# Kernel tuning notes

Hardware: AMD Instinct MI355X
Metric: run time of the kernel (lower is better)

The kernel has to match this reference:

```python
import jax, jax.numpy as jnp
import numpy as np

B, H, S = 64, 1024, 512
MIN_VAL, MAX_VAL = -1.0, 1.0
EPS = 1e-8  # torch F.cosine_similarity default eps


def setup_inputs() -> dict:
    key = jax.random.key(0)
    k1, k2, k3 = jax.random.split(key, 3)
    tree_state = jax.random.normal(k1, (B, H), dtype=jnp.float32)
    seq_states = jax.random.normal(k2, (B, H, S), dtype=jnp.float32)
    # binary validity mask (float, as it is multiplied in)
    seq_mask = (jax.random.uniform(k3, (B, S)) < 0.9).astype(jnp.float32)
    return {"tree_state": tree_state, "seq_states": seq_states, "seq_mask": seq_mask}


def reference(tree_state, seq_states, seq_mask):
    # scan over the seq axis; carry h: (B, H)
    xs = (jnp.transpose(seq_states, (2, 0, 1)), seq_mask.T)  # (S,B,H), (S,B)

    def step(h, x):
        s, m = x  # s: (B,H), m: (B,)
        dot = jnp.sum(h * s, axis=-1)  # (B,)
        denom = jnp.maximum(
            jnp.linalg.norm(h, axis=-1) * jnp.linalg.norm(s, axis=-1), EPS
        )
        cos = (dot / denom)[:, None]  # (B,1)
        h_new = jnp.clip(h + (s - h * cos) * m[:, None], MIN_VAL, MAX_VAL)
        return h_new, None

    h, _ = jax.lax.scan(step, tree_state, xs)
    return h
```

## Files before the change

kernel.cpp:

```cpp
#include <hip/hip_runtime.h>


#define NB 64
#define NH 1024
#define NS 512

typedef float v4f __attribute__((ext_vector_type(4)));
typedef int v4i __attribute__((ext_vector_type(4)));

template <int N> struct ic { static constexpr int value = N; };

template <int CTRL>
__device__ __forceinline__ float dpp_add(float x) {
  int s = __builtin_amdgcn_update_dpp(0, __builtin_bit_cast(int, x), CTRL, 0xf,
                                      0xf, true);
  return x + __builtin_bit_cast(float, s);
}

__device__ __forceinline__ float readlane_f(float v, int lane) {
  return __builtin_bit_cast(
      float, __builtin_amdgcn_readlane(__builtin_bit_cast(int, v), lane));
}

__device__ __forceinline__ void wave_sum3(float& a, float& b, float& c) {
  a = dpp_add<0x111>(a); b = dpp_add<0x111>(b); c = dpp_add<0x111>(c);
  a = dpp_add<0x112>(a); b = dpp_add<0x112>(b); c = dpp_add<0x112>(c);
  a = dpp_add<0x114>(a); b = dpp_add<0x114>(b); c = dpp_add<0x114>(c);
  a = dpp_add<0x118>(a); b = dpp_add<0x118>(b); c = dpp_add<0x118>(c);
  a = dpp_add<0x142>(a); b = dpp_add<0x142>(b); c = dpp_add<0x142>(c);
  a = dpp_add<0x143>(a); b = dpp_add<0x143>(b); c = dpp_add<0x143>(c);
  a = readlane_f(a, 63);
  b = readlane_f(b, 63);
  c = readlane_f(c, 63);
}

#define GLD4(dst, p, OFFSTR)                                   \
  asm volatile("global_load_dwordx4 %0, %1, off" OFFSTR        \
               : "=v"(dst)                                     \
               : "v"(p))
#define GLD1(dst, p)                                           \
  asm volatile("global_load_dword %0, %1, off" : "=v"(dst) : "v"(p))

template <int IMM>
__device__ __forceinline__ void dsr128(v4f& d, unsigned a) {
  asm volatile("ds_read_b128 %[d], %[a] offset:%[o]"
               : [d] "=v"(d)
               : [a] "v"(a), [o] "n"(IMM));
}
template <int IMM>
__device__ __forceinline__ void dsw32(unsigned a, float v) {
  asm volatile("ds_write_b32 %[a], %[v] offset:%[o]" ::[a] "v"(a), [v] "v"(v),
               [o] "n"(IMM));
}
__device__ __forceinline__ void bld4(v4f& d, unsigned voff, v4i srsrc,
                                     unsigned so) {
  asm volatile("buffer_load_dwordx4 %[d], %[vo], %[rs], %[so] offen"
               : [d] "=v"(d)
               : [vo] "v"(voff), [rs] "s"(srsrc), [so] "s"(so));
}

#define VMW12(rg)                                                          \
  asm volatile("s_waitcnt vmcnt(12)"                                       \
               : "+v"((rg)[0]), "+v"((rg)[1]), "+v"((rg)[2]), "+v"((rg)[3]))
#define LGK0(sv)                                                           \
  asm volatile("s_waitcnt lgkmcnt(0)"                                      \
               : "+v"((sv)[0]), "+v"((sv)[1]), "+v"((sv)[2]), "+v"((sv)[3]))

template <int T>
__device__ __forceinline__ void read_issue(unsigned rb, v4f (&sv)[4]) {
  dsr128<T * 4096 + 0>(sv[0], rb);
  dsr128<T * 4096 + 1024>(sv[1], rb);
  dsr128<T * 4096 + 2048>(sv[2], rb);
  dsr128<T * 4096 + 3072>(sv[3], rb);
}

template <int S>
__device__ __forceinline__ void stage_write(unsigned wb, v4f (&rg)[4]) {
#define DSWUJ(u, j) dsw32<(j) * 4096 + 256 * S + 64 * (u)>(wb, rg[u][j])
  DSWUJ(0, 0); DSWUJ(0, 1); DSWUJ(0, 2); DSWUJ(0, 3);
  DSWUJ(1, 0); DSWUJ(1, 1); DSWUJ(1, 2); DSWUJ(1, 3);
  DSWUJ(2, 0); DSWUJ(2, 1); DSWUJ(2, 2); DSWUJ(2, 3);
  DSWUJ(3, 0); DSWUJ(3, 1); DSWUJ(3, 2); DSWUJ(3, 3);
#undef DSWUJ
}

__device__ __forceinline__ void stage_load(v4f (&rg)[4], unsigned voff,
                                           v4i srsrc, unsigned& so) {
  bld4(rg[0], voff, srsrc, so); so += 32768u;
  bld4(rg[1], voff, srsrc, so); so += 32768u;
  bld4(rg[2], voff, srsrc, so); so += 32768u;
  bld4(rg[3], voff, srsrc, so); so += 32768u;
}

__device__ __forceinline__ void compute_step(float (&h)[16],
                                             const v4f (&sv)[4]) {
  float d0 = 0.f, d1 = 0.f, d2 = 0.f, d3 = 0.f;
  float e0 = 0.f, e1 = 0.f, e2 = 0.f, e3 = 0.f;
  float f0 = 0.f, f1 = 0.f, f2 = 0.f, f3 = 0.f;
#pragma unroll
  for (int m = 0; m < 4; ++m) {
    const float s0 = sv[m][0], s1 = sv[m][1], s2 = sv[m][2], s3 = sv[m][3];
    d0 = fmaf(h[4 * m + 0], s0, d0);
    e0 = fmaf(h[4 * m + 0], h[4 * m + 0], e0);
    f0 = fmaf(s0, s0, f0);
    d1 = fmaf(h[4 * m + 1], s1, d1);
    e1 = fmaf(h[4 * m + 1], h[4 * m + 1], e1);
    f1 = fmaf(s1, s1, f1);
    d2 = fmaf(h[4 * m + 2], s2, d2);
    e2 = fmaf(h[4 * m + 2], h[4 * m + 2], e2);
    f2 = fmaf(s2, s2, f2);
    d3 = fmaf(h[4 * m + 3], s3, d3);
    e3 = fmaf(h[4 * m + 3], h[4 * m + 3], e3);
    f3 = fmaf(s3, s3, f3);
  }
  float dot = (d0 + d1) + (d2 + d3);
  float hh = (e0 + e1) + (e2 + e3);
  float ss = (f0 + f1) + (f2 + f3);
  wave_sum3(dot, hh, ss);
  const float p = fmaxf(hh * ss, 1e-16f);
  const float c = dot * __builtin_amdgcn_rsqf(p);
  const float a = 1.0f - c;
#pragma unroll
  for (int m = 0; m < 4; ++m) {
    h[4 * m + 0] =
        __builtin_amdgcn_fmed3f(fmaf(h[4 * m + 0], a, sv[m][0]), -1.0f, 1.0f);
    h[4 * m + 1] =
        __builtin_amdgcn_fmed3f(fmaf(h[4 * m + 1], a, sv[m][1]), -1.0f, 1.0f);
    h[4 * m + 2] =
        __builtin_amdgcn_fmed3f(fmaf(h[4 * m + 2], a, sv[m][2]), -1.0f, 1.0f);
    h[4 * m + 3] =
        __builtin_amdgcn_fmed3f(fmaf(h[4 * m + 3], a, sv[m][3]), -1.0f, 1.0f);
  }
}

__global__ __launch_bounds__(64, 1) void otsu_scan_kernel(
    const float* __restrict__ tree,
    const float* __restrict__ seq,
    const float* __restrict__ mask,
    float* __restrict__ out) {
  __shared__ float lds[2 * 16 * 1024];
  const int b = blockIdx.x;
  const int l = threadIdx.x;

  const float* hrow = tree + b * NH + 4 * l;
  v4f hv[4];
  GLD4(hv[0], hrow, "");
  GLD4(hv[1], hrow, " offset:1024");
  GLD4(hv[2], hrow, " offset:2048");
  GLD4(hv[3], hrow, " offset:3072");
  float m8[8];
  {
    const float* mp = mask + b * NS + l;
    GLD1(m8[0], mp);
    GLD1(m8[1], mp + 64);
    GLD1(m8[2], mp + 128);
    GLD1(m8[3], mp + 192);
    GLD1(m8[4], mp + 256);
    GLD1(m8[5], mp + 320);
    GLD1(m8[6], mp + 384);
    GLD1(m8[7], mp + 448);
  }
  asm volatile("s_waitcnt vmcnt(0)"
               : "+v"(hv[0]), "+v"(hv[1]), "+v"(hv[2]), "+v"(hv[3]),
                 "+v"(m8[0]), "+v"(m8[1]), "+v"(m8[2]), "+v"(m8[3]),
                 "+v"(m8[4]), "+v"(m8[5]), "+v"(m8[6]), "+v"(m8[7]));

  float h[16];
#pragma unroll
  for (int m = 0; m < 4; ++m) {
    h[4 * m + 0] = hv[m][0];
    h[4 * m + 1] = hv[m][1];
    h[4 * m + 2] = hv[m][2];
    h[4 * m + 3] = hv[m][3];
  }

  unsigned mbits = 0u;
#pragma unroll
  for (int i = 0; i < 8; ++i)
    if (m8[i] != 0.0f) mbits |= (1u << i);

  if (!(__builtin_amdgcn_readlane((int)mbits, 0) & 1)) {
#pragma unroll
    for (int i = 0; i < 16; ++i)
      h[i] = __builtin_amdgcn_fmed3f(h[i], -1.0f, 1.0f);
  }

  v4i srsrc;
  {
    const unsigned long long base =
        (unsigned long long)(seq + (size_t)b * NH * NS);
    srsrc[0] = (int)(unsigned)(base & 0xffffffffull);
    srsrc[1] = (int)(unsigned)(base >> 32);
    srsrc[2] = NH * NS * 4;
    srsrc[3] = 0x00020000;
  }
  const unsigned voff = (unsigned)((l >> 2) * 2048 + (l & 3) * 16);
  const unsigned lb = (unsigned)(unsigned long long)(&lds[0]);
  const unsigned rb0 = lb + 16u * (unsigned)l;
  const unsigned wb0 = lb + (unsigned)((l & 3) * 16384 + (l >> 2) * 4);
  unsigned so = 0u;

  v4f ring[8][4];
  v4f sval[2][4];

  stage_load(ring[0], voff, srsrc, so);
  stage_load(ring[1], voff, srsrc, so);
  stage_load(ring[2], voff, srsrc, so);
  stage_load(ring[3], voff, srsrc, so);
#define PSTEP(v)                                              \
  do {                                                        \
    VMW12(ring[(v) & 7]);                                     \
    stage_write<(v)>(wb0, ring[(v) & 7]);                     \
    stage_load(ring[((v) + 4) & 7], voff, srsrc, so);         \
    if ((v) == 11) so -= 2097088u;     \
  } while (0)
  PSTEP(0);  PSTEP(1);  PSTEP(2);  PSTEP(3);
  PSTEP(4);  PSTEP(5);  PSTEP(6);  PSTEP(7);
  PSTEP(8);  PSTEP(9);  PSTEP(10); PSTEP(11);
  PSTEP(12); PSTEP(13); PSTEP(14); PSTEP(15);
#undef PSTEP

  read_issue<0>(rb0, sval[0]);

  unsigned rb_cur = rb0;
  unsigned wb_cur = wb0 ^ 0x10000u;

#pragma unroll 1
  for (int g = 0; g < 32; ++g) {
    const int lbase = (16 * g) & 63;
    const int msh = g >> 2;
    auto step = [&](auto sc) {
      constexpr int S = decltype(sc)::value;
      LGK0(sval[S & 1]);
      if constexpr (S < 15) read_issue<S + 1>(rb_cur, sval[(S + 1) & 1]);
      const unsigned mw =
          (unsigned)__builtin_amdgcn_readlane((int)mbits, lbase + S);
      if ((mw >> msh) & 1u) compute_step(h, sval[S & 1]);
      VMW12(ring[S & 7]);
      stage_write<S>(wb_cur, ring[S & 7]);
      stage_load(ring[(S + 4) & 7], voff, srsrc, so);
      if constexpr (S == 11) { so -= 2097088u; }
      if constexpr (S == 15) { read_issue<0>(rb_cur ^ 0x10000u, sval[0]); }
    };
    step(ic<0>{});  step(ic<1>{});  step(ic<2>{});  step(ic<3>{});
    step(ic<4>{});  step(ic<5>{});  step(ic<6>{});  step(ic<7>{});
    step(ic<8>{});  step(ic<9>{});  step(ic<10>{}); step(ic<11>{});
    step(ic<12>{}); step(ic<13>{}); step(ic<14>{}); step(ic<15>{});
    rb_cur ^= 0x10000u;
    wb_cur ^= 0x10000u;
  }

  asm volatile("s_waitcnt vmcnt(0) lgkmcnt(0)" ::: "memory");

  float* orow = out + b * NH + 4 * l;
#pragma unroll
  for (int m = 0; m < 4; ++m) {
    float4 v;
    v.x = h[4 * m + 0];
    v.y = h[4 * m + 1];
    v.z = h[4 * m + 2];
    v.w = h[4 * m + 3];
    *(float4*)(orow + 256 * m) = v;
  }
}

extern "C" void kernel_launch(void* const* d_in, const int* in_sizes, int n_in,
                              void* d_out, int out_size, void* d_ws,
                              size_t ws_size, hipStream_t stream) {
  const float* tree = (const float*)d_in[0];
  const float* seq = (const float*)d_in[1];
  const float* mask = (const float*)d_in[2];
  float* out = (float*)d_out;
  otsu_scan_kernel<<<dim3(NB), dim3(64), 0, stream>>>(tree, seq, mask, out);
}
```

Measured before the change: 316.4 us.

## Split each batch row across four waves with LDS cross-wave reduction

Each block now runs four waves instead of one, and each wave owns a quarter of the hidden dimension (4 floats per lane instead of 16). The per-step dot and norm partials are reduced inside each wave with DPP, exchanged through LDS, and synchronised with a block barrier each step. Streaming now uses global loads instead of buffer loads, and the wait thresholds are adjusted. This aims to cut the per-wave serial compute and memory issue on the latency-bound scan, at the cost of a barrier and an extra LDS round trip on every sequence step.

```diff
diff --git a/kernel.cpp b/kernel.cpp
--- a/kernel.cpp
+++ b/kernel.cpp
@@ -6,7 +6,6 @@
 #define NS 512
 
 typedef float v4f __attribute__((ext_vector_type(4)));
-typedef int v4i __attribute__((ext_vector_type(4)));
 
 template <int N> struct ic { static constexpr int value = N; };
 
@@ -17,28 +16,18 @@
   return x + __builtin_bit_cast(float, s);
 }
 
-__device__ __forceinline__ float readlane_f(float v, int lane) {
-  return __builtin_bit_cast(
-      float, __builtin_amdgcn_readlane(__builtin_bit_cast(int, v), lane));
-}
-
-__device__ __forceinline__ void wave_sum3(float& a, float& b, float& c) {
+__device__ __forceinline__ void wave_red3_to63(float& a, float& b, float& c) {
   a = dpp_add<0x111>(a); b = dpp_add<0x111>(b); c = dpp_add<0x111>(c);
   a = dpp_add<0x112>(a); b = dpp_add<0x112>(b); c = dpp_add<0x112>(c);
   a = dpp_add<0x114>(a); b = dpp_add<0x114>(b); c = dpp_add<0x114>(c);
   a = dpp_add<0x118>(a); b = dpp_add<0x118>(b); c = dpp_add<0x118>(c);
   a = dpp_add<0x142>(a); b = dpp_add<0x142>(b); c = dpp_add<0x142>(c);
   a = dpp_add<0x143>(a); b = dpp_add<0x143>(b); c = dpp_add<0x143>(c);
-  a = readlane_f(a, 63);
-  b = readlane_f(b, 63);
-  c = readlane_f(c, 63);
-}
-
-#define GLD4(dst, p, OFFSTR)                                   \
-  asm volatile("global_load_dwordx4 %0, %1, off" OFFSTR        \
-               : "=v"(dst)                                     \
-               : "v"(p))
-#define GLD1(dst, p)                                           \
+}
+
+#define GLD4(dst, p) \
+  asm volatile("global_load_dwordx4 %0, %1, off" : "=v"(dst) : "v"(p))
+#define GLD1(dst, p) \
   asm volatile("global_load_dword %0, %1, off" : "=v"(dst) : "v"(p))
 
 template <int IMM>
@@ -52,102 +41,35 @@
   asm volatile("ds_write_b32 %[a], %[v] offset:%[o]" ::[a] "v"(a), [v] "v"(v),
                [o] "n"(IMM));
 }
-__device__ __forceinline__ void bld4(v4f& d, unsigned voff, v4i srsrc,
-                                     unsigned so) {
-  asm volatile("buffer_load_dwordx4 %[d], %[vo], %[rs], %[so] offen"
-               : [d] "=v"(d)
-               : [vo] "v"(voff), [rs] "s"(srsrc), [so] "s"(so));
-}
-
-#define VMW12(rg)                                                          \
-  asm volatile("s_waitcnt vmcnt(12)"                                       \
-               : "+v"((rg)[0]), "+v"((rg)[1]), "+v"((rg)[2]), "+v"((rg)[3]))
-#define LGK0(sv)                                                           \
-  asm volatile("s_waitcnt lgkmcnt(0)"                                      \
-               : "+v"((sv)[0]), "+v"((sv)[1]), "+v"((sv)[2]), "+v"((sv)[3]))
-
-template <int T>
-__device__ __forceinline__ void read_issue(unsigned rb, v4f (&sv)[4]) {
-  dsr128<T * 4096 + 0>(sv[0], rb);
-  dsr128<T * 4096 + 1024>(sv[1], rb);
-  dsr128<T * 4096 + 2048>(sv[2], rb);
-  dsr128<T * 4096 + 3072>(sv[3], rb);
-}
+
+#define VMW3(r) asm volatile("s_waitcnt vmcnt(3)" : "+v"(r))
+#define LGK0SV(sv) asm volatile("s_waitcnt lgkmcnt(0)" : "+v"(sv))
+#define LGK5PR(p0, p1, p2)                  \
+  asm volatile("s_waitcnt lgkmcnt(5)"       \
+               : "+v"(p0), "+v"(p1), "+v"(p2))
 
 template <int S>
-__device__ __forceinline__ void stage_write(unsigned wb, v4f (&rg)[4]) {
-#define DSWUJ(u, j) dsw32<(j) * 4096 + 256 * S + 64 * (u)>(wb, rg[u][j])
-  DSWUJ(0, 0); DSWUJ(0, 1); DSWUJ(0, 2); DSWUJ(0, 3);
-  DSWUJ(1, 0); DSWUJ(1, 1); DSWUJ(1, 2); DSWUJ(1, 3);
-  DSWUJ(2, 0); DSWUJ(2, 1); DSWUJ(2, 2); DSWUJ(2, 3);
-  DSWUJ(3, 0); DSWUJ(3, 1); DSWUJ(3, 2); DSWUJ(3, 3);
-#undef DSWUJ
-}
-
-__device__ __forceinline__ void stage_load(v4f (&rg)[4], unsigned voff,
-                                           v4i srsrc, unsigned& so) {
-  bld4(rg[0], voff, srsrc, so); so += 32768u;
-  bld4(rg[1], voff, srsrc, so); so += 32768u;
-  bld4(rg[2], voff, srsrc, so); so += 32768u;
-  bld4(rg[3], voff, srsrc, so); so += 32768u;
-}
-
-__device__ __forceinline__ void compute_step(float (&h)[16],
-                                             const v4f (&sv)[4]) {
-  float d0 = 0.f, d1 = 0.f, d2 = 0.f, d3 = 0.f;
-  float e0 = 0.f, e1 = 0.f, e2 = 0.f, e3 = 0.f;
-  float f0 = 0.f, f1 = 0.f, f2 = 0.f, f3 = 0.f;
-#pragma unroll
-  for (int m = 0; m < 4; ++m) {
-    const float s0 = sv[m][0], s1 = sv[m][1], s2 = sv[m][2], s3 = sv[m][3];
-    d0 = fmaf(h[4 * m + 0], s0, d0);
-    e0 = fmaf(h[4 * m + 0], h[4 * m + 0], e0);
-    f0 = fmaf(s0, s0, f0);
-    d1 = fmaf(h[4 * m + 1], s1, d1);
-    e1 = fmaf(h[4 * m + 1], h[4 * m + 1], e1);
-    f1 = fmaf(s1, s1, f1);
-    d2 = fmaf(h[4 * m + 2], s2, d2);
-    e2 = fmaf(h[4 * m + 2], h[4 * m + 2], e2);
-    f2 = fmaf(s2, s2, f2);
-    d3 = fmaf(h[4 * m + 3], s3, d3);
-    e3 = fmaf(h[4 * m + 3], h[4 * m + 3], e3);
-    f3 = fmaf(s3, s3, f3);
-  }
-  float dot = (d0 + d1) + (d2 + d3);
-  float hh = (e0 + e1) + (e2 + e3);
-  float ss = (f0 + f1) + (f2 + f3);
-  wave_sum3(dot, hh, ss);
-  const float p = fmaxf(hh * ss, 1e-16f);
-  const float c = dot * __builtin_amdgcn_rsqf(p);
-  const float a = 1.0f - c;
-#pragma unroll
-  for (int m = 0; m < 4; ++m) {
-    h[4 * m + 0] =
-        __builtin_amdgcn_fmed3f(fmaf(h[4 * m + 0], a, sv[m][0]), -1.0f, 1.0f);
-    h[4 * m + 1] =
-        __builtin_amdgcn_fmed3f(fmaf(h[4 * m + 1], a, sv[m][1]), -1.0f, 1.0f);
-    h[4 * m + 2] =
-        __builtin_amdgcn_fmed3f(fmaf(h[4 * m + 2], a, sv[m][2]), -1.0f, 1.0f);
-    h[4 * m + 3] =
-        __builtin_amdgcn_fmed3f(fmaf(h[4 * m + 3], a, sv[m][3]), -1.0f, 1.0f);
-  }
-}
-
-__global__ __launch_bounds__(64, 1) void otsu_scan_kernel(
+__device__ __forceinline__ void stage_write(unsigned wb, v4f rg) {
+  dsw32<0 * 4096 + 64 * S>(wb, rg[0]);
+  dsw32<1 * 4096 + 64 * S>(wb, rg[1]);
+  dsw32<2 * 4096 + 64 * S>(wb, rg[2]);
+  dsw32<3 * 4096 + 64 * S>(wb, rg[3]);
+}
+
+__global__ __launch_bounds__(256, 1) void otsu_scan_kernel(
     const float* __restrict__ tree,
     const float* __restrict__ seq,
     const float* __restrict__ mask,
     float* __restrict__ out) {
-  __shared__ float lds[2 * 16 * 1024];
+  __shared__ float lds[2 * 16 * 1024 + 64];
   const int b = blockIdx.x;
-  const int l = threadIdx.x;
-
-  const float* hrow = tree + b * NH + 4 * l;
-  v4f hv[4];
-  GLD4(hv[0], hrow, "");
-  GLD4(hv[1], hrow, " offset:1024");
-  GLD4(hv[2], hrow, " offset:2048");
-  GLD4(hv[3], hrow, " offset:3072");
+  const int tid = threadIdx.x;
+  const int w = tid >> 6;
+  const int l = tid & 63;
+
+  const float* hrow = tree + b * NH + 256 * w + 4 * l;
+  v4f h;
+  GLD4(h, hrow);
   float m8[8];
   {
     const float* mp = mask + b * NS + l;
@@ -161,18 +83,8 @@
     GLD1(m8[7], mp + 448);
   }
   asm volatile("s_waitcnt vmcnt(0)"
-               : "+v"(hv[0]), "+v"(hv[1]), "+v"(hv[2]), "+v"(hv[3]),
-                 "+v"(m8[0]), "+v"(m8[1]), "+v"(m8[2]), "+v"(m8[3]),
+               : "+v"(h), "+v"(m8[0]), "+v"(m8[1]), "+v"(m8[2]), "+v"(m8[3]),
                  "+v"(m8[4]), "+v"(m8[5]), "+v"(m8[6]), "+v"(m8[7]));
-
-  float h[16];
-#pragma unroll
-  for (int m = 0; m < 4; ++m) {
-    h[4 * m + 0] = hv[m][0];
-    h[4 * m + 1] = hv[m][1];
-    h[4 * m + 2] = hv[m][2];
-    h[4 * m + 3] = hv[m][3];
-  }
 
   unsigned mbits = 0u;
 #pragma unroll
@@ -181,49 +93,45 @@
 
   if (!(__builtin_amdgcn_readlane((int)mbits, 0) & 1)) {
 #pragma unroll
-    for (int i = 0; i < 16; ++i)
+    for (int i = 0; i < 4; ++i)
       h[i] = __builtin_amdgcn_fmed3f(h[i], -1.0f, 1.0f);
   }
 
-  v4i srsrc;
-  {
-    const unsigned long long base =
-        (unsigned long long)(seq + (size_t)b * NH * NS);
-    srsrc[0] = (int)(unsigned)(base & 0xffffffffull);
-    srsrc[1] = (int)(unsigned)(base >> 32);
-    srsrc[2] = NH * NS * 4;
-    srsrc[3] = 0x00020000;
-  }
-  const unsigned voff = (unsigned)((l >> 2) * 2048 + (l & 3) * 16);
+  const float* sp0 = seq + (size_t)b * NH * NS + (size_t)w * 131072 +
+                     (l >> 2) * 512 + (l & 3) * 4;
+  const float* sp = sp0;
   const unsigned lb = (unsigned)(unsigned long long)(&lds[0]);
-  const unsigned rb0 = lb + 16u * (unsigned)l;
-  const unsigned wb0 = lb + (unsigned)((l & 3) * 16384 + (l >> 2) * 4);
-  unsigned so = 0u;
-
-  v4f ring[8][4];
-  v4f sval[2][4];
-
-  stage_load(ring[0], voff, srsrc, so);
-  stage_load(ring[1], voff, srsrc, so);
-  stage_load(ring[2], voff, srsrc, so);
-  stage_load(ring[3], voff, srsrc, so);
-#define PSTEP(v)                                              \
-  do {                                                        \
-    VMW12(ring[(v) & 7]);                                     \
-    stage_write<(v)>(wb0, ring[(v) & 7]);                     \
-    stage_load(ring[((v) + 4) & 7], voff, srsrc, so);         \
-    if ((v) == 11) so -= 2097088u;     \
+  unsigned rb = lb + 1024u * (unsigned)w + 16u * (unsigned)l;
+  unsigned wbase =
+      lb + 16384u * (unsigned)(l & 3) + 1024u * (unsigned)w +
+      4u * (unsigned)(l >> 2);
+  const unsigned vp = lb + 131072u + 4u * (unsigned)w;
+  const unsigned pb = lb + 131072u;
+
+  v4f ring[8];
+  v4f sval[2];
+
+  GLD4(ring[0], sp); sp += 8192;
+  GLD4(ring[1], sp); sp += 8192;
+  GLD4(ring[2], sp); sp += 8192;
+  GLD4(ring[3], sp); sp += 8192;
+#define PCH(c)                                              \
+  do {                                                      \
+    VMW3(ring[(c) & 7]);                                    \
+    stage_write<(c)>(wbase, ring[(c) & 7]);                 \
+    if ((c) == 12) sp -= 131056;     \
+    GLD4(ring[((c) + 4) & 7], sp);                          \
+    sp += 8192;                                             \
   } while (0)
-  PSTEP(0);  PSTEP(1);  PSTEP(2);  PSTEP(3);
-  PSTEP(4);  PSTEP(5);  PSTEP(6);  PSTEP(7);
-  PSTEP(8);  PSTEP(9);  PSTEP(10); PSTEP(11);
-  PSTEP(12); PSTEP(13); PSTEP(14); PSTEP(15);
-#undef PSTEP
-
-  read_issue<0>(rb0, sval[0]);
-
-  unsigned rb_cur = rb0;
-  unsigned wb_cur = wb0 ^ 0x10000u;
+  PCH(0);  PCH(1);  PCH(2);  PCH(3);
+  PCH(4);  PCH(5);  PCH(6);  PCH(7);
+  PCH(8);  PCH(9);  PCH(10); PCH(11);
+  PCH(12); PCH(13); PCH(14); PCH(15);
+#undef PCH
+
+  dsr128<0>(sval[0], rb);
+
+  unsigned wb = wbase ^ 0x10000u;
 
 #pragma unroll 1
   for (int g = 0; g < 32; ++g) {
@@ -231,37 +139,72 @@
     const int msh = g >> 2;
     auto step = [&](auto sc) {
       constexpr int S = decltype(sc)::value;
-      LGK0(sval[S & 1]);
-      if constexpr (S < 15) read_issue<S + 1>(rb_cur, sval[(S + 1) & 1]);
+      LGK0SV(sval[S & 1]);
       const unsigned mw =
           (unsigned)__builtin_amdgcn_readlane((int)mbits, lbase + S);
-      if ((mw >> msh) & 1u) compute_step(h, sval[S & 1]);
-      VMW12(ring[S & 7]);
-      stage_write<S>(wb_cur, ring[S & 7]);
-      stage_load(ring[(S + 4) & 7], voff, srsrc, so);
-      if constexpr (S == 11) { so -= 2097088u; }
-      if constexpr (S == 15) { read_issue<0>(rb_cur ^ 0x10000u, sval[0]); }
+      const bool act = (mw >> msh) & 1u;
+      v4f pr0, pr1, pr2;
+      if (act) {
+        const v4f s = sval[S & 1];
+        float pd0 = h[0] * s[0]; pd0 = fmaf(h[1], s[1], pd0);
+        float pd1 = h[2] * s[2]; pd1 = fmaf(h[3], s[3], pd1);
+        float ph0 = h[0] * h[0]; ph0 = fmaf(h[1], h[1], ph0);
+        float ph1 = h[2] * h[2]; ph1 = fmaf(h[3], h[3], ph1);
+        float ps0 = s[0] * s[0]; ps0 = fmaf(s[1], s[1], ps0);
+        float ps1 = s[2] * s[2]; ps1 = fmaf(s[3], s[3], ps1);
+        float pd = pd0 + pd1, ph = ph0 + ph1, ps = ps0 + ps1;
+        wave_red3_to63(pd, ph, ps);
+        if (l == 63) {
+          dsw32<(S & 3) * 64 + 0>(vp, pd);
+          dsw32<(S & 3) * 64 + 16>(vp, ph);
+          dsw32<(S & 3) * 64 + 32>(vp, ps);
+        }
+        asm volatile("s_waitcnt lgkmcnt(0)" ::: "memory");
+      }
+      asm volatile("s_barrier" ::: "memory");
+      if (act) {
+        dsr128<(S & 3) * 64 + 0>(pr0, pb);
+        dsr128<(S & 3) * 64 + 16>(pr1, pb);
+        dsr128<(S & 3) * 64 + 32>(pr2, pb);
+      }
+      VMW3(ring[S & 7]);
+      stage_write<S>(wb, ring[S & 7]);
+      if constexpr (S == 12) sp = (g < 30) ? sp - 131056 : sp0;
+      GLD4(ring[(S + 4) & 7], sp);
+      sp += 8192;
+      if constexpr (S < 15) dsr128<(S + 1) * 4096>(sval[(S + 1) & 1], rb);
+      else                  dsr128<0>(sval[0], rb ^ 0x10000u);
+      if (act) {
+        LGK5PR(pr0, pr1, pr2);
+        float dot = (pr0[0] + pr0[1]) + (pr0[2] + pr0[3]);
+        float hh = (pr1[0] + pr1[1]) + (pr1[2] + pr1[3]);
+        float ss = (pr2[0] + pr2[1]) + (pr2[2] + pr2[3]);
+        const float p = fmaxf(hh * ss, 1e-16f);
+        const float c = dot * __builtin_amdgcn_rsqf(p);
+        const float a = 1.0f - c;
+        const v4f s = sval[S & 1];
+#pragma unroll
+        for (int i = 0; i < 4; ++i)
+          h[i] = __builtin_amdgcn_fmed3f(fmaf(h[i], a, s[i]), -1.0f, 1.0f);
+      }
     };
     step(ic<0>{});  step(ic<1>{});  step(ic<2>{});  step(ic<3>{});
     step(ic<4>{});  step(ic<5>{});  step(ic<6>{});  step(ic<7>{});
     step(ic<8>{});  step(ic<9>{});  step(ic<10>{}); step(ic<11>{});
     step(ic<12>{}); step(ic<13>{}); step(ic<14>{}); step(ic<15>{});
-    rb_cur ^= 0x10000u;
-    wb_cur ^= 0x10000u;
+    rb ^= 0x10000u;
+    wb ^= 0x10000u;
   }
 
   asm volatile("s_waitcnt vmcnt(0) lgkmcnt(0)" ::: "memory");
 
-  float* orow = out + b * NH + 4 * l;
-#pragma unroll
-  for (int m = 0; m < 4; ++m) {
-    float4 v;
-    v.x = h[4 * m + 0];
-    v.y = h[4 * m + 1];
-    v.z = h[4 * m + 2];
-    v.w = h[4 * m + 3];
-    *(float4*)(orow + 256 * m) = v;
-  }
+  float* orow = out + b * NH + 256 * w + 4 * l;
+  float4 v;
+  v.x = h[0];
+  v.y = h[1];
+  v.z = h[2];
+  v.w = h[3];
+  *(float4*)orow = v;
 }
 
 extern "C" void kernel_launch(void* const* d_in, const int* in_sizes, int n_in,
@@ -271,5 +214,5 @@
   const float* seq = (const float*)d_in[1];
   const float* mask = (const float*)d_in[2];
   float* out = (float*)d_out;
-  otsu_scan_kernel<<<dim3(NB), dim3(64), 0, stream>>>(tree, seq, mask, out);
-}
+  otsu_scan_kernel<<<dim3(NB), dim3(256), 0, stream>>>(tree, seq, mask, out);
+}
```

After: 310.7 us. About the same (-1.8%).
